# Kernel optimization log

Measured on AMD Instinct MI355X. Metric: run time of the kernel, lower is better.

Reference implementation:

```python
import jax, jax.numpy as jnp
import numpy as np

DIM, N_HEADS, N_KV, HEAD_DIM = 4096, 32, 8, 128
N_REP = N_HEADS // N_KV
MAX_BS, MAX_SEQ = 2, 2048
ROPE_THETA = 500000.0


def setup_inputs() -> dict:
    key = jax.random.key(0)
    ks = jax.random.split(key, 6)
    b, s = 2, 2048
    x = jax.random.normal(ks[0], (b, s, DIM), dtype=jnp.float32)
    # weights stored like nn.Linear: [out, in]
    sc = 1.0 / np.sqrt(DIM)
    wq = jax.random.normal(ks[1], (N_HEADS * HEAD_DIM, DIM), dtype=jnp.float32) * sc
    wk = jax.random.normal(ks[2], (N_KV * HEAD_DIM, DIM), dtype=jnp.float32) * sc
    wv = jax.random.normal(ks[3], (N_KV * HEAD_DIM, DIM), dtype=jnp.float32) * sc
    wo = jax.random.normal(ks[4], (DIM, N_HEADS * HEAD_DIM), dtype=jnp.float32) * sc
    # rotary tables (real/imag of freq_complex)
    t = jnp.arange(s, dtype=jnp.float32)
    inv = ROPE_THETA ** (-jnp.arange(0, HEAD_DIM, 2, dtype=jnp.float32) / HEAD_DIM)
    ang = t[:, None] * inv[None, :]  # [s, head_dim/2]
    freqs_cos = jnp.cos(ang)
    freqs_sin = jnp.sin(ang)
    cache_k = jnp.zeros((MAX_BS, MAX_SEQ, N_KV, HEAD_DIM), dtype=jnp.float32)
    cache_v = jnp.zeros((MAX_BS, MAX_SEQ, N_KV, HEAD_DIM), dtype=jnp.float32)
    return {"x": x, "wq": wq, "wk": wk, "wv": wv, "wo": wo,
            "freqs_cos": freqs_cos, "freqs_sin": freqs_sin,
            "cache_k": cache_k, "cache_v": cache_v, "start_pos": 0}


def _apply_rope(t, cos, sin):
    # t: [b, s, h, hd]; complex rotation over adjacent pairs
    b, s, h, hd = t.shape
    t2 = t.reshape(b, s, h, hd // 2, 2)
    t0, t1 = t2[..., 0], t2[..., 1]
    c = cos[None, :, None, :]
    sn = sin[None, :, None, :]
    o0 = t0 * c - t1 * sn
    o1 = t0 * sn + t1 * c
    return jnp.stack([o0, o1], axis=-1).reshape(b, s, h, hd)


def reference(x, wq, wk, wv, wo, freqs_cos, freqs_sin, cache_k, cache_v, start_pos):
    b, s, _ = x.shape
    xq = (x @ wq.T).reshape(b, s, N_HEADS, HEAD_DIM)
    xk = (x @ wk.T).reshape(b, s, N_KV, HEAD_DIM)
    xv = (x @ wv.T).reshape(b, s, N_KV, HEAD_DIM)
    xq = _apply_rope(xq, freqs_cos, freqs_sin)
    xk = _apply_rope(xk, freqs_cos, freqs_sin)
    # KV-cache append at start_pos
    cache_k = jax.lax.dynamic_update_slice(cache_k, xk, (0, start_pos, 0, 0))
    cache_v = jax.lax.dynamic_update_slice(cache_v, xv, (0, start_pos, 0, 0))
    kv_len = start_pos + s
    keys = cache_k[:b, :kv_len]   # [b, kv, n_kv, hd]
    vals = cache_v[:b, :kv_len]
    # GQA: group query heads instead of repeating K/V (same math as repeat_kv)
    q = xq.reshape(b, s, N_KV, N_REP, HEAD_DIM)
    scores = jnp.einsum('bsgrd,btgd->bgrst', q, keys) / np.sqrt(HEAD_DIM)
    # causal mask: query i (absolute pos start_pos+i) attends to j <= start_pos+i
    qpos = start_pos + jnp.arange(s)
    kpos = jnp.arange(kv_len)
    mask = kpos[None, :] <= qpos[:, None]  # [s, kv]
    scores = jnp.where(mask[None, None, None], scores, -jnp.inf)
    probs = jax.nn.softmax(scores, axis=-1)
    out = jnp.einsum('bgrst,btgd->bsgrd', probs, vals).reshape(b, s, N_HEADS * HEAD_DIM)
    return out @ wo.T
```

## Files before the change

### kernel.cpp

```cpp
#include <hip/hip_runtime.h>
#include <stdint.h>

typedef unsigned short ushort_t;
typedef short v8s __attribute__((ext_vector_type(8)));
typedef short v4s __attribute__((ext_vector_type(4)));
typedef float v4f __attribute__((ext_vector_type(4)));
typedef unsigned int uint32;

#define DIM   4096
#define NH    32
#define NKV   8
#define HD    128
#define SEQ   2048
#define BATCH 2
#define NTOK  (BATCH * SEQ)
#define QKVN  (NH * HD + 2 * NKV * HD)
#define KOFF  (NH * HD)
#define VOFF  (NH * HD + NKV * HD)

__device__ __forceinline__ ushort_t f2bf(float f) {
    uint32 u = __float_as_uint(f);
    u += 0x7fff + ((u >> 16) & 1);
    return (ushort_t)(u >> 16);
}
__device__ __forceinline__ float bf2f(ushort_t h) {
    return __uint_as_float(((uint32)h) << 16);
}
__device__ __forceinline__ void gl2lds16(const void* g, void* l) {
    __builtin_amdgcn_global_load_lds(
        (const __attribute__((address_space(1))) uint32*)g,
        (__attribute__((address_space(3))) uint32*)l, 16, 0, 0);
}
#if __has_builtin(__builtin_amdgcn_exp2f)
__device__ __forceinline__ float fast_exp2(float x) { return __builtin_amdgcn_exp2f(x); }
#else
__device__ __forceinline__ float fast_exp2(float x) { return exp2f(x); }
#endif

#if !defined(__HIP_DEVICE_COMPILE__)
__host__ __device__ static inline v4f MFMA_B16_K16(v4s a, v4s b, v4f c) {
    (void)a; (void)b; return c;
}
#elif __has_builtin(__builtin_amdgcn_mfma_f32_16x16x16_bf16)
#define MFMA_B16_K16(A, B, C) __builtin_amdgcn_mfma_f32_16x16x16_bf16(A, B, C, 0, 0, 0)
#elif __has_builtin(__builtin_amdgcn_mfma_f32_16x16x16bf16_1k)
#define MFMA_B16_K16(A, B, C) __builtin_amdgcn_mfma_f32_16x16x16bf16_1k(A, B, C, 0, 0, 0)
#else
#error "no 16x16x16 bf16 MFMA builtin on device"
#endif

__global__ void cvt_f32_bf16(const float* __restrict__ src,
                             ushort_t* __restrict__ dst, int n4) {
    int i = blockIdx.x * blockDim.x + threadIdx.x;
    if (i >= n4) return;
    float4 v = ((const float4*)src)[i];
    uint32 lo = ((uint32)f2bf(v.y) << 16) | f2bf(v.x);
    uint32 hi = ((uint32)f2bf(v.w) << 16) | f2bf(v.z);
    ((uint2*)dst)[i] = make_uint2(lo, hi);
}

template <int OUT_BF16>
__global__ __launch_bounds__(512, 2) void gemm_bt8(const ushort_t* __restrict__ A,
                                                   const ushort_t* __restrict__ B,
                                                   float* __restrict__ Cf,
                                                   ushort_t* __restrict__ Cb,
                                                   int M, int N, int K) {
    __shared__ ushort_t sm[2][2][16384];
    const int t = threadIdx.x;
    const int w = t >> 6, lane = t & 63;
    const int g8 = lane >> 4, l16 = lane & 15;
    const int wr = w >> 2, wc = w & 3;

    const int gx = gridDim.x;
    const int nwg = gx * gridDim.y;
    const int wg0 = blockIdx.y * gx + blockIdx.x;
    const int swz = (wg0 & 7) * (nwg >> 3) + (wg0 >> 3);
    const int bm = swz % gx, bn = swz / gx;

    const ushort_t* Ab = A + (size_t)bm * 256 * K;
    const ushort_t* Bb = B + (size_t)bn * 256 * K;

    const int prt = t >> 3;
    const int gg  = (t & 7) ^ (prt & 7);
    const int rA0 = prt,                              rA1 = prt + 128;
    const int rB0 = ((prt >> 5) << 6) + (prt & 31),   rB1 = rB0 + 128;

    const int pgk  = g8 ^ (l16 & 7);
    const int aoff = (wr * 64 + l16) * 64;
    const int boff = (wc * 32 + l16) * 64;

#define STAGE_A(buf, ah, k0)                                                   \
  do {                                                                         \
    gl2lds16(&Ab[(size_t)(rA0 + (ah) * 64) * K + (k0) + gg * 8],               \
             &sm[buf][0][(ah) * 8192 + t * 8]);                                \
    gl2lds16(&Ab[(size_t)(rA1 + (ah) * 64) * K + (k0) + gg * 8],               \
             &sm[buf][0][(ah) * 8192 + 4096 + t * 8]);                         \
  } while (0)
#define STAGE_B(buf, bh, k0)                                                   \
  do {                                                                         \
    gl2lds16(&Bb[(size_t)(rB0 + (bh) * 32) * K + (k0) + gg * 8],               \
             &sm[buf][1][(bh) * 8192 + t * 8]);                                \
    gl2lds16(&Bb[(size_t)(rB1 + (bh) * 32) * K + (k0) + gg * 8],               \
             &sm[buf][1][(bh) * 8192 + 4096 + t * 8]);                         \
  } while (0)
#define LD_A(dst, buf, ihi)                                                    \
  do {                                                                         \
    _Pragma("unroll") for (int i_ = 0; i_ < 4; ++i_) {                         \
      (dst)[i_ * 2 + 0] = *(const v8s*)&sm[buf][0][(ihi) * 8192 + aoff + i_ * 1024 + pgk * 8];       \
      (dst)[i_ * 2 + 1] = *(const v8s*)&sm[buf][0][(ihi) * 8192 + aoff + i_ * 1024 + (pgk ^ 4) * 8]; \
    }                                                                          \
  } while (0)
#define LD_B(dst, buf, jhi)                                                    \
  do {                                                                         \
    _Pragma("unroll") for (int j_ = 0; j_ < 2; ++j_) {                         \
      (dst)[j_ * 2 + 0] = *(const v8s*)&sm[buf][1][(jhi) * 8192 + boff + j_ * 1024 + pgk * 8];       \
      (dst)[j_ * 2 + 1] = *(const v8s*)&sm[buf][1][(jhi) * 8192 + boff + j_ * 1024 + (pgk ^ 4) * 8]; \
    }                                                                          \
  } while (0)
#define MM(IHI, JHI, AF, BF)                                                   \
  do {                                                                         \
    __builtin_amdgcn_s_setprio(1);                                             \
    _Pragma("unroll") for (int k_ = 0; k_ < 2; ++k_)                           \
      _Pragma("unroll") for (int i_ = 0; i_ < 4; ++i_)                         \
        _Pragma("unroll") for (int j_ = 0; j_ < 2; ++j_)                       \
          acc[(IHI) * 4 + i_][(JHI) * 2 + j_] =                                \
              __builtin_amdgcn_mfma_f32_16x16x32_bf16(                         \
                  (AF)[i_ * 2 + k_], (BF)[j_ * 2 + k_],                        \
                  acc[(IHI) * 4 + i_][(JHI) * 2 + j_], 0, 0, 0);               \
    __builtin_amdgcn_s_setprio(0);                                             \
  } while (0)

#define TILE_BODY(T, BF, BL, BH)                                               \
  do {                                                                         \
    const int Tp1 = (T) + 1, Tp2 = (T) + 2;                                    \
              \
    LD_A(af, BF, 0);                                                           \
    LD_B(BH, BF, 1);                                                           \
    if (Tp1 < nk) STAGE_B((BF) ^ 1, 1, Tp1 << 6);                              \
    MM(0, 0, af, BL);                                                          \
    __builtin_amdgcn_s_barrier();                                              \
                                             \
    if (Tp2 < nk) STAGE_A(BF, 0, Tp2 << 6);                                    \
    MM(0, 1, af, BH);                                                          \
    __builtin_amdgcn_s_barrier();                                              \
                                             \
    LD_A(af, BF, 1);                                                           \
    if (Tp2 < nk) STAGE_B(BF, 0, Tp2 << 6);                                    \
    MM(1, 1, af, BH);                                                          \
    __builtin_amdgcn_s_barrier();                                              \
          \
    if (Tp2 < nk) STAGE_A(BF, 1, Tp2 << 6);                                    \
    if ((T) < nk - 2) { asm volatile("s_waitcnt vmcnt(6)" ::: "memory"); }     \
    else              { asm volatile("s_waitcnt vmcnt(0)" ::: "memory"); }     \
    __builtin_amdgcn_s_barrier();                                              \
    if (Tp1 < nk) LD_B(BH, (BF) ^ 1, 0);     \
    MM(1, 0, af, BL);                                                          \
            \
  } while (0)

    v4f acc[8][4];
    v4f z = {0.f, 0.f, 0.f, 0.f};
#pragma unroll
    for (int i = 0; i < 8; i++)
#pragma unroll
        for (int j = 0; j < 4; j++) acc[i][j] = z;
    v8s af[8], b0[4], b1[4];

    const int nk = K >> 6;

    STAGE_A(0, 0, 0);  STAGE_B(0, 0, 0);  STAGE_A(0, 1, 0);  STAGE_B(0, 1, 0);
    STAGE_A(1, 0, 64); STAGE_B(1, 0, 64); STAGE_A(1, 1, 64);
    asm volatile("s_waitcnt vmcnt(6)" ::: "memory");
    __builtin_amdgcn_s_barrier();
    LD_B(b0, 0, 0);

    for (int T = 0; T < nk; T += 2) {
        TILE_BODY(T, 0, b0, b1);
        TILE_BODY(T + 1, 1, b1, b0);
    }

#undef STAGE_A
#undef STAGE_B
#undef LD_A
#undef LD_B
#undef MM
#undef TILE_BODY

    const int rowb = bm * 256 + wr * 128;
    const int colb = bn * 256 + wc * 64;
#pragma unroll
    for (int i = 0; i < 8; i++)
#pragma unroll
        for (int j = 0; j < 4; j++)
#pragma unroll
            for (int r = 0; r < 4; r++) {
                int row = rowb + i * 16 + g8 * 4 + r;
                int col = colb + j * 16 + l16;
                float v = acc[i][j][r];
                if (OUT_BF16)
                    Cb[(size_t)row * N + col] = f2bf(v);
                else
                    Cf[(size_t)row * N + col] = v;
            }
}

__global__ __launch_bounds__(256) void rope_reorg(const ushort_t* __restrict__ qkv,
                                                  const float* __restrict__ fc,
                                                  const float* __restrict__ fs,
                                                  ushort_t* __restrict__ Qo,
                                                  ushort_t* __restrict__ Ko) {
    const int tok = blockIdx.x;
    const int bb = tok >> 11, s = tok & 2047;
    const ushort_t* base = qkv + (size_t)tok * QKVN;
    const int t = threadIdx.x;
    const float qscale = 0.08838834764831845f * 1.4426950408889634f;
    uint32* Qw = (uint32*)Qo;
    uint32* Kw = (uint32*)Ko;
#pragma unroll
    for (int i = 0; i < 8; ++i) {
        int p = i * 256 + t;
        int hh = p >> 6, pi = p & 63;
        float c = fc[s * 64 + pi], sn = fs[s * 64 + pi];
        uint32 u = *(const uint32*)&base[hh * 128 + 2 * pi];
        float t0 = bf2f((ushort_t)(u & 0xffff));
        float t1 = bf2f((ushort_t)(u >> 16));
        float o0 = (t0 * c - t1 * sn) * qscale;
        float o1 = (t0 * sn + t1 * c) * qscale;
        size_t dst = (((size_t)bb * NH + hh) * SEQ + s) * HD + 2 * pi;
        Qw[dst >> 1] = ((uint32)f2bf(o1) << 16) | f2bf(o0);
    }
#pragma unroll
    for (int i = 0; i < 2; ++i) {
        int p = i * 256 + t;
        int hh = p >> 6, pi = p & 63;
        float c = fc[s * 64 + pi], sn = fs[s * 64 + pi];
        uint32 u = *(const uint32*)&base[KOFF + hh * 128 + 2 * pi];
        float t0 = bf2f((ushort_t)(u & 0xffff));
        float t1 = bf2f((ushort_t)(u >> 16));
        float o0 = t0 * c - t1 * sn;
        float o1 = t0 * sn + t1 * c;
        size_t dst = (((size_t)bb * NKV + hh) * SEQ + s) * HD + 2 * pi;
        Kw[dst >> 1] = ((uint32)f2bf(o1) << 16) | f2bf(o0);
    }
}

__global__ __launch_bounds__(256) void v_transpose(const ushort_t* __restrict__ qkv,
                                                   ushort_t* __restrict__ Vt) {
    __shared__ ushort_t tile[64][136];
    const int st = blockIdx.x, kvh = blockIdx.y, bb = blockIdx.z;
    const int t = threadIdx.x;
    const int s0 = st * 64;
#pragma unroll
    for (int i = 0; i < 4; ++i) {
        int c = i * 256 + t;
        int r = c >> 4, col8 = (c & 15) * 8;
        int tok = (bb << 11) + s0 + r;
        *(v8s*)&tile[r][col8] =
            *(const v8s*)&qkv[(size_t)tok * QKVN + VOFF + kvh * 128 + col8];
    }
    __syncthreads();
#pragma unroll
    for (int i = 0; i < 4; ++i) {
        int c = i * 256 + t;
        int d = c >> 3, s8 = (c & 7) * 8;
        ushort_t tmp[8];
#pragma unroll
        for (int j = 0; j < 8; j++) tmp[j] = tile[s8 + j][d];
        *(v8s*)&Vt[(((size_t)bb * NKV + kvh) * HD + d) * SEQ + s0 + s8] =
            *(v8s*)tmp;
    }
}

__global__ __launch_bounds__(512, 4) void attn_kernel(const ushort_t* __restrict__ Q,
                                                      const ushort_t* __restrict__ Kc,
                                                      const ushort_t* __restrict__ Vt,
                                                      ushort_t* __restrict__ Out) {
    __shared__ ushort_t Ks[2][64 * 128];
    __shared__ ushort_t Vs[2][128 * 64];
    const int qtb = gridDim.x - 1 - blockIdx.x;
    const int h = blockIdx.y, bb = blockIdx.z;
    const int kvh = h >> 2;
    const int t = threadIdx.x, w = t >> 6, lane = t & 63;
    const int g8 = lane >> 4, l16 = lane & 15;
    const int R = qtb * 128 + w * 16;
    const int qrow = R + l16;

    const size_t qb = (((size_t)bb * NH + h) * SEQ + R) * HD;
    v8s qf[4];
#pragma unroll
    for (int ks = 0; ks < 4; ++ks)
        qf[ks] = *(const v8s*)&Q[qb + (size_t)l16 * HD + ks * 32 + g8 * 8];

    float m_i = -3.0e38f, l_i = 0.f;
    v4f z = {0.f, 0.f, 0.f, 0.f};
    v4f o[8];
#pragma unroll
    for (int n = 0; n < 8; n++) o[n] = z;

    const ushort_t* Kbase = Kc + ((size_t)bb * NKV + kvh) * SEQ * HD;
    const ushort_t* Vbase = Vt + ((size_t)bb * NKV + kvh) * HD * SEQ;

#define STAGE_KV(bf, kt)                                                       \
  do {                                                                         \
    const ushort_t* Kt_ = Kbase + (size_t)(kt) * 64 * HD;                      \
    _Pragma("unroll") for (int i_ = 0; i_ < 2; ++i_) {                         \
      int c_ = i_ * 512 + t;                                                   \
      int r_ = c_ >> 4, cc_ = (c_ & 15) ^ (r_ & 15);                           \
      gl2lds16(&Kt_[r_ * 128 + cc_ * 8], &Ks[bf][c_ * 8]);                     \
    }                                                                          \
    _Pragma("unroll") for (int i_ = 0; i_ < 2; ++i_) {                         \
      int c_ = i_ * 512 + t;                                                   \
      int d_ = c_ >> 3, cc_ = (c_ & 7) ^ (d_ & 7);                             \
      gl2lds16(&Vbase[(size_t)d_ * SEQ + (kt) * 64 + cc_ * 8],                 \
               &Vs[bf][c_ * 8]);                                               \
    }                                                                          \
  } while (0)

    const int nkt = 2 * qtb + 2;
    STAGE_KV(0, 0);
    for (int kt = 0; kt < nkt; ++kt) {
        const int bf = kt & 1;
        const int k0 = kt * 64;
        if (kt + 1 < nkt) {
            STAGE_KV(bf ^ 1, kt + 1);
            asm volatile("s_waitcnt vmcnt(4)" ::: "memory");
        } else {
            asm volatile("s_waitcnt vmcnt(0)" ::: "memory");
        }
        __builtin_amdgcn_s_barrier();

        v4f s[4];
#pragma unroll
        for (int j = 0; j < 4; j++) s[j] = z;
        __builtin_amdgcn_s_setprio(1);
#pragma unroll
        for (int j = 0; j < 4; j++)
#pragma unroll
            for (int ks = 0; ks < 4; ks++) {
                const v8s kb = *(const v8s*)&Ks[bf][((j * 16 + l16) * 16 + ((ks * 4 + g8) ^ l16)) * 8];
                s[j] = __builtin_amdgcn_mfma_f32_16x16x32_bf16(kb, qf[ks], s[j], 0, 0, 0);
            }
        __builtin_amdgcn_s_setprio(0);

        if (kt >= 2 * qtb) {
#pragma unroll
            for (int j = 0; j < 4; j++)
#pragma unroll
                for (int r = 0; r < 4; r++) {
                    int key = k0 + j * 16 + g8 * 4 + r;
                    if (key > qrow) s[j][r] = -3.0e38f;
                }
        }

        float mx = fmaxf(fmaxf(s[0][0], s[0][1]), fmaxf(s[0][2], s[0][3]));
#pragma unroll
        for (int j = 1; j < 4; j++)
            mx = fmaxf(mx, fmaxf(fmaxf(s[j][0], s[j][1]), fmaxf(s[j][2], s[j][3])));
        mx = fmaxf(mx, __shfl_xor(mx, 16, 64));
        mx = fmaxf(mx, __shfl_xor(mx, 32, 64));
        float mnew = fmaxf(m_i, mx);
        float alpha = fast_exp2(m_i - mnew);
        m_i = mnew;

        float sum = 0.f;
        v4s pj[4];
#pragma unroll
        for (int j = 0; j < 4; j++)
#pragma unroll
            for (int r = 0; r < 4; r++) {
                float p = fast_exp2(s[j][r] - m_i);
                sum += p;
                pj[j][r] = (short)f2bf(p);
            }
        sum += __shfl_xor(sum, 16, 64);
        sum += __shfl_xor(sum, 32, 64);
        l_i = l_i * alpha + sum;

        float alo[4];
#pragma unroll
        for (int r = 0; r < 4; r++) alo[r] = __shfl(alpha, g8 * 4 + r, 64);
#pragma unroll
        for (int n = 0; n < 8; n++)
#pragma unroll
            for (int r = 0; r < 4; r++) o[n][r] *= alo[r];

        __builtin_amdgcn_s_setprio(1);
#pragma unroll
        for (int j = 0; j < 4; j++)
#pragma unroll
            for (int n = 0; n < 8; n++) {
                const int d = n * 16 + l16;
                const v4s vb = *(const v4s*)&Vs[bf][d * 64 + (((j * 2 + (g8 >> 1)) ^ (l16 & 7)) * 8) + (g8 & 1) * 4];
                o[n] = MFMA_B16_K16(pj[j], vb, o[n]);
            }
        __builtin_amdgcn_s_setprio(0);

        __builtin_amdgcn_s_barrier();
    }
#undef STAGE_KV

    float lo[4];
#pragma unroll
    for (int r = 0; r < 4; r++) lo[r] = __shfl(l_i, g8 * 4 + r, 64);
#pragma unroll
    for (int n = 0; n < 8; n++)
#pragma unroll
        for (int r = 0; r < 4; r++) {
            int row = R + g8 * 4 + r;
            int col = n * 16 + l16;
            Out[(((size_t)bb * SEQ + row) * NH + h) * HD + col] = f2bf(o[n][r] / lo[r]);
        }
}

extern "C" void kernel_launch(void* const* d_in, const int* in_sizes, int n_in,
                              void* d_out, int out_size, void* d_ws, size_t ws_size,
                              hipStream_t stream) {
    const float* x  = (const float*)d_in[0];
    const float* wq = (const float*)d_in[1];
    const float* wk = (const float*)d_in[2];
    const float* wv = (const float*)d_in[3];
    const float* wo = (const float*)d_in[4];
    const float* fc = (const float*)d_in[5];
    const float* fs = (const float*)d_in[6];
    float* out = (float*)d_out;

    ushort_t* ws = (ushort_t*)d_ws;
    size_t off = 0;
    ushort_t* xb    = ws + off; off += (size_t)NTOK * DIM;
    ushort_t* wqkvb = ws + off; off += (size_t)QKVN * DIM;
    ushort_t* wob   = ws + off; off += (size_t)DIM * DIM;
    ushort_t* qkv   = ws + off; off += (size_t)NTOK * QKVN;
    ushort_t* Qb    = ws + off; off += (size_t)BATCH * NH * SEQ * HD;
    ushort_t* Kb    = ws + off; off += (size_t)BATCH * NKV * SEQ * HD;
    ushort_t* Vt    = ws + off; off += (size_t)BATCH * NKV * HD * SEQ;
    ushort_t* attn_out = xb;

    cvt_f32_bf16<<<(NTOK * DIM / 4) / 256, 256, 0, stream>>>(x, xb, NTOK * DIM / 4);
    cvt_f32_bf16<<<(DIM * DIM / 4) / 256, 256, 0, stream>>>(wq, wqkvb, DIM * DIM / 4);
    cvt_f32_bf16<<<(NKV * HD * DIM / 4) / 256, 256, 0, stream>>>(
        wk, wqkvb + (size_t)KOFF * DIM, NKV * HD * DIM / 4);
    cvt_f32_bf16<<<(NKV * HD * DIM / 4) / 256, 256, 0, stream>>>(
        wv, wqkvb + (size_t)VOFF * DIM, NKV * HD * DIM / 4);
    cvt_f32_bf16<<<(DIM * DIM / 4) / 256, 256, 0, stream>>>(wo, wob, DIM * DIM / 4);

    dim3 g1(NTOK / 256, QKVN / 256);
    gemm_bt8<1><<<g1, 512, 0, stream>>>(xb, wqkvb, nullptr, qkv, NTOK, QKVN, DIM);

    rope_reorg<<<NTOK, 256, 0, stream>>>(qkv, fc, fs, Qb, Kb);
    dim3 gv(SEQ / 64, NKV, BATCH);
    v_transpose<<<gv, 256, 0, stream>>>(qkv, Vt);

    dim3 ga(SEQ / 128, NH, BATCH);
    attn_kernel<<<ga, 512, 0, stream>>>(Qb, Kb, Vt, attn_out);

    dim3 g2(NTOK / 256, DIM / 256);
    gemm_bt8<0><<<g2, 512, 0, stream>>>(attn_out, wob, out, nullptr, NTOK, DIM, DIM);
}
```

Before: 790.1 us.

## Software-pipeline attention PV matmul one tile behind QK with triple-buffered V

Restructures the flash-attention loop so the P·V MFMAs for the previous key tile run right after the current tile's QK^T MFMAs, giving the scheduler independent matrix work to overlap with the softmax. V is triple-buffered in LDS to support the lag. It also adds a lazy rescale that skips updating the running max and rescaling O when the max grows by at most 8 (log2 units), and precomputes the LDS addresses. In exchange the kernel uses more LDS, which may lower occupancy, and it adds a prologue wait that serializes the first tile's load.

```diff
diff --git a/kernel.cpp b/kernel.cpp
--- a/kernel.cpp
+++ b/kernel.cpp
@@ -275,8 +275,8 @@
                                                       const ushort_t* __restrict__ Kc,
                                                       const ushort_t* __restrict__ Vt,
                                                       ushort_t* __restrict__ Out) {
-    __shared__ ushort_t Ks[2][64 * 128];
-    __shared__ ushort_t Vs[2][128 * 64];
+    __shared__ ushort_t Ks[2 * 64 * 128];
+    __shared__ ushort_t Vs[3 * 128 * 64];
     const int qtb = gridDim.x - 1 - blockIdx.x;
     const int h = blockIdx.y, bb = blockIdx.z;
     const int kvh = h >> 2;
@@ -291,38 +291,58 @@
     for (int ks = 0; ks < 4; ++ks)
         qf[ks] = *(const v8s*)&Q[qb + (size_t)l16 * HD + ks * 32 + g8 * 8];
 
+    int kadr[4], vadr[4];
+#pragma unroll
+    for (int ks = 0; ks < 4; ++ks)
+        kadr[ks] = l16 * 128 + (((ks * 4 + g8) ^ l16)) * 8;
+#pragma unroll
+    for (int j = 0; j < 4; ++j)
+        vadr[j] = l16 * 64 + (((j * 2 + (g8 >> 1)) ^ (l16 & 7)) * 8) + (g8 & 1) * 4;
+
     float m_i = -3.0e38f, l_i = 0.f;
     v4f z = {0.f, 0.f, 0.f, 0.f};
     v4f o[8];
 #pragma unroll
     for (int n = 0; n < 8; n++) o[n] = z;
 
+    v4s pjp[4];
+    float alo_p[4] = {1.f, 1.f, 1.f, 1.f};
+    int skip_p = 1;
+
     const ushort_t* Kbase = Kc + ((size_t)bb * NKV + kvh) * SEQ * HD;
     const ushort_t* Vbase = Vt + ((size_t)bb * NKV + kvh) * HD * SEQ;
 
-#define STAGE_KV(bf, kt)                                                       \
+#define STAGE_K(kb, kt)                                                        \
   do {                                                                         \
     const ushort_t* Kt_ = Kbase + (size_t)(kt) * 64 * HD;                      \
     _Pragma("unroll") for (int i_ = 0; i_ < 2; ++i_) {                         \
       int c_ = i_ * 512 + t;                                                   \
       int r_ = c_ >> 4, cc_ = (c_ & 15) ^ (r_ & 15);                           \
-      gl2lds16(&Kt_[r_ * 128 + cc_ * 8], &Ks[bf][c_ * 8]);                     \
+      gl2lds16(&Kt_[r_ * 128 + cc_ * 8], &Ks[(kb) * 8192 + c_ * 8]);           \
     }                                                                          \
+  } while (0)
+#define STAGE_V(vb, kt)                                                        \
+  do {                                                                         \
     _Pragma("unroll") for (int i_ = 0; i_ < 2; ++i_) {                         \
       int c_ = i_ * 512 + t;                                                   \
       int d_ = c_ >> 3, cc_ = (c_ & 7) ^ (d_ & 7);                             \
       gl2lds16(&Vbase[(size_t)d_ * SEQ + (kt) * 64 + cc_ * 8],                 \
-               &Vs[bf][c_ * 8]);                                               \
+               &Vs[(vb) * 8192 + c_ * 8]);                                     \
     }                                                                          \
   } while (0)
 
     const int nkt = 2 * qtb + 2;
-    STAGE_KV(0, 0);
+    STAGE_K(0, 0); STAGE_V(0, 0);
+    asm volatile("s_waitcnt vmcnt(0)" ::: "memory");
+    __builtin_amdgcn_s_barrier();
+
     for (int kt = 0; kt < nkt; ++kt) {
-        const int bf = kt & 1;
+        const int kb = kt & 1;
+        const int vbp = (kt + 2) % 3;
         const int k0 = kt * 64;
         if (kt + 1 < nkt) {
-            STAGE_KV(bf ^ 1, kt + 1);
+            STAGE_K(kb ^ 1, kt + 1);
+            STAGE_V((kt + 1) % 3, kt + 1);
             asm volatile("s_waitcnt vmcnt(4)" ::: "memory");
         } else {
             asm volatile("s_waitcnt vmcnt(0)" ::: "memory");
@@ -337,10 +357,28 @@
         for (int j = 0; j < 4; j++)
 #pragma unroll
             for (int ks = 0; ks < 4; ks++) {
-                const v8s kb = *(const v8s*)&Ks[bf][((j * 16 + l16) * 16 + ((ks * 4 + g8) ^ l16)) * 8];
-                s[j] = __builtin_amdgcn_mfma_f32_16x16x32_bf16(kb, qf[ks], s[j], 0, 0, 0);
+                const v8s kb_ = *(const v8s*)&Ks[kb * 8192 + j * 2048 + kadr[ks]];
+                s[j] = __builtin_amdgcn_mfma_f32_16x16x32_bf16(kb_, qf[ks], s[j], 0, 0, 0);
             }
         __builtin_amdgcn_s_setprio(0);
+
+        if (kt) {
+            if (!skip_p) {
+#pragma unroll
+                for (int n = 0; n < 8; n++)
+#pragma unroll
+                    for (int r = 0; r < 4; r++) o[n][r] *= alo_p[r];
+            }
+            __builtin_amdgcn_s_setprio(1);
+#pragma unroll
+            for (int j = 0; j < 4; j++)
+#pragma unroll
+                for (int n = 0; n < 8; n++) {
+                    const v4s vb_ = *(const v4s*)&Vs[vbp * 8192 + n * 1024 + vadr[j]];
+                    o[n] = MFMA_B16_K16(pjp[j], vb_, o[n]);
+                }
+            __builtin_amdgcn_s_setprio(0);
+        }
 
         if (kt >= 2 * qtb) {
 #pragma unroll
@@ -358,46 +396,55 @@
             mx = fmaxf(mx, fmaxf(fmaxf(s[j][0], s[j][1]), fmaxf(s[j][2], s[j][3])));
         mx = fmaxf(mx, __shfl_xor(mx, 16, 64));
         mx = fmaxf(mx, __shfl_xor(mx, 32, 64));
-        float mnew = fmaxf(m_i, mx);
-        float alpha = fast_exp2(m_i - mnew);
-        m_i = mnew;
+
+        const int skip = __all(mx - m_i <= 8.0f);
+        float alpha = 1.f;
+        if (!skip) {
+            float mnew = fmaxf(m_i, mx);
+            alpha = fast_exp2(m_i - mnew);
+            m_i = mnew;
+        }
 
         float sum = 0.f;
-        v4s pj[4];
 #pragma unroll
         for (int j = 0; j < 4; j++)
 #pragma unroll
             for (int r = 0; r < 4; r++) {
                 float p = fast_exp2(s[j][r] - m_i);
                 sum += p;
-                pj[j][r] = (short)f2bf(p);
+                pjp[j][r] = (short)f2bf(p);
             }
         sum += __shfl_xor(sum, 16, 64);
         sum += __shfl_xor(sum, 32, 64);
         l_i = l_i * alpha + sum;
 
-        float alo[4];
-#pragma unroll
-        for (int r = 0; r < 4; r++) alo[r] = __shfl(alpha, g8 * 4 + r, 64);
-#pragma unroll
-        for (int n = 0; n < 8; n++)
-#pragma unroll
-            for (int r = 0; r < 4; r++) o[n][r] *= alo[r];
-
-        __builtin_amdgcn_s_setprio(1);
+        if (!skip) {
+#pragma unroll
+            for (int r = 0; r < 4; r++) alo_p[r] = __shfl(alpha, g8 * 4 + r, 64);
+        }
+        skip_p = skip;
+
+        __builtin_amdgcn_s_barrier();
+    }
+
+    {
+        const int vbl = (nkt + 2) % 3;
+        if (!skip_p) {
+#pragma unroll
+            for (int n = 0; n < 8; n++)
+#pragma unroll
+                for (int r = 0; r < 4; r++) o[n][r] *= alo_p[r];
+        }
 #pragma unroll
         for (int j = 0; j < 4; j++)
 #pragma unroll
             for (int n = 0; n < 8; n++) {
-                const int d = n * 16 + l16;
-                const v4s vb = *(const v4s*)&Vs[bf][d * 64 + (((j * 2 + (g8 >> 1)) ^ (l16 & 7)) * 8) + (g8 & 1) * 4];
-                o[n] = MFMA_B16_K16(pj[j], vb, o[n]);
+                const v4s vb_ = *(const v4s*)&Vs[vbl * 8192 + n * 1024 + vadr[j]];
+                o[n] = MFMA_B16_K16(pjp[j], vb_, o[n]);
             }
-        __builtin_amdgcn_s_setprio(0);
-
-        __builtin_amdgcn_s_barrier();
-    }
-#undef STAGE_KV
+    }
+#undef STAGE_K
+#undef STAGE_V
 
     float lo[4];
 #pragma unroll
```

After: 782.4 us. Within noise of the previous version (-1.0%).
